# Kernel optimization log

Measured on AMD Instinct MI355X. Metric: run time of the kernel, lower is better.

Reference implementation:

```python
import jax, jax.numpy as jnp
import numpy as np

IN, HID, BATCH = 1024, 1024, 4096


def _linear_params(key, out_dim, in_dim):
    # torch.nn.Linear default init: U(-1/sqrt(in), 1/sqrt(in))
    k1, k2 = jax.random.split(key)
    bound = 1.0 / np.sqrt(in_dim)
    w = jax.random.uniform(k1, (out_dim, in_dim), jnp.float32, -bound, bound)
    b = jax.random.uniform(k2, (out_dim,), jnp.float32, -bound, bound)
    return w, b


def setup_inputs() -> dict:
    key = jax.random.key(0)
    keys = jax.random.split(key, 11)
    inp = {
        'input': jax.random.normal(keys[0], (BATCH, IN), jnp.float32),
        'h': jax.random.normal(keys[1], (BATCH, HID), jnp.float32),
        'c': jax.random.normal(keys[2], (BATCH, HID), jnp.float32),
    }
    names = ['i_i', 'i_h', 'f_i', 'f_h', 'g_i', 'g_h', 'o_i', 'o_h']
    for n, k in zip(names, keys[3:]):
        in_dim = IN if n.endswith('_i') else HID
        w, b = _linear_params(k, HID, in_dim)
        inp['w_' + n] = w
        inp['b_' + n] = b
    return inp


def reference(input, h, c,
              w_i_i, b_i_i, w_i_h, b_i_h,
              w_f_i, b_f_i, w_f_h, b_f_h,
              w_g_i, b_g_i, w_g_h, b_g_h,
              w_o_i, b_o_i, w_o_h, b_o_h):
    def lin(x, w, b):
        return x @ w.T + b

    i = jax.nn.sigmoid(lin(input, w_i_i, b_i_i) + lin(h, w_i_h, b_i_h))
    f = jax.nn.sigmoid(lin(input, w_f_i, b_f_i) + lin(h, w_f_h, b_f_h))
    g = jnp.tanh(lin(input, w_g_i, b_g_i) + lin(h, w_g_h, b_g_h))
    o = jax.nn.sigmoid(lin(input, w_o_i, b_o_i) + lin(h, w_o_h, b_o_h))
    c_prime = f * c + i * g
    h_prime = o * jnp.tanh(c_prime)
    return (h_prime, c_prime)
```

## Files before the change

kernel.cpp:

```cpp
#include <hip/hip_runtime.h>
#include <stdint.h>

#define BATCH 4096
#define IN_DIM 1024
#define HID 1024
#define KDIM 2048
#define NGATE 4096
#define EPITCH 136

typedef __attribute__((ext_vector_type(4))) float floatx4;
typedef __attribute__((ext_vector_type(8))) __bf16 bf16x8;
typedef __attribute__((ext_vector_type(8))) unsigned short ushort8;

__device__ __forceinline__ unsigned short f2bf(float f) {
    union { float f; unsigned int u; } v; v.f = f;
    unsigned int u = v.u;
    u += 0x7fffu + ((u >> 16) & 1u);
    return (unsigned short)(u >> 16);
}
__device__ __forceinline__ float bf2f(unsigned short s) {
    union { unsigned int u; float f; } v; v.u = ((unsigned int)s) << 16;
    return v.f;
}
__device__ __forceinline__ ushort8 cvt8(const float* __restrict__ src) {
    float4 v0 = ((const float4*)src)[0];
    float4 v1 = ((const float4*)src)[1];
    ushort8 o = { f2bf(v0.x), f2bf(v0.y), f2bf(v0.z), f2bf(v0.w),
                  f2bf(v1.x), f2bf(v1.y), f2bf(v1.z), f2bf(v1.w) };
    return o;
}

__global__ __launch_bounds__(256) void prep_kernel(
    const float* __restrict__ x,  const float* __restrict__ h,
    const float* __restrict__ wii, const float* __restrict__ wih,
    const float* __restrict__ wfi, const float* __restrict__ wfh,
    const float* __restrict__ wgi, const float* __restrict__ wgh,
    const float* __restrict__ woi, const float* __restrict__ woh,
    const float* __restrict__ bii, const float* __restrict__ bih,
    const float* __restrict__ bfi, const float* __restrict__ bfh,
    const float* __restrict__ bgi, const float* __restrict__ bgh,
    const float* __restrict__ boi, const float* __restrict__ boh,
    unsigned short* __restrict__ Xb,
    unsigned short* __restrict__ Wb,
    float* __restrict__ bias)
{
    const int bid = blockIdx.x;
    const int tid = threadIdx.x;

    if (bid < 2048) {
        const int e = (bid * 256 + tid) * 8;
        const int b = e >> 10, k = e & 1023;
        *(ushort8*)(Xb + (size_t)b * KDIM + k) = cvt8(x + e);
    } else if (bid < 4096) {
        const int e = ((bid - 2048) * 256 + tid) * 8;
        const int b = e >> 10, k = e & 1023;
        *(ushort8*)(Xb + (size_t)b * KDIM + 1024 + k) = cvt8(h + e);
    } else if (bid < 8192) {
        const int m   = (bid - 4096) >> 9;
        const int off = (bid - 4096) & 511;
        const int e = (off * 256 + tid) * 8;
        const int n = e >> 10, k = e & 1023;
        const float* src;
        switch (m) {
            case 0: src = wii; break; case 1: src = wih; break;
            case 2: src = wfi; break; case 3: src = wfh; break;
            case 4: src = wgi; break; case 5: src = wgh; break;
            case 6: src = woi; break; default: src = woh; break;
        }
        const int gate = m >> 1, part = m & 1;
        *(ushort8*)(Wb + (size_t)(n * 4 + gate) * KDIM + part * 1024 + k)
            = cvt8(src + e);
    } else {
        const int t = (bid - 8192) * 256 + tid;
        const int gate = (bid - 8192) >> 2;
        const int n = t & 1023;
        const float *bi, *bh_;
        switch (gate) {
            case 0: bi = bii; bh_ = bih; break;
            case 1: bi = bfi; bh_ = bfh; break;
            case 2: bi = bgi; bh_ = bgh; break;
            default: bi = boi; bh_ = boh; break;
        }
        bias[n * 4 + gate] = bi[n] + bh_[n];
    }
}

#define GLD16(g, l)                                                          \
    __builtin_amdgcn_global_load_lds(                                        \
        (__attribute__((address_space(1))) void*)(g),                        \
        (__attribute__((address_space(3))) void*)(l), 16, 0, 0)

__global__ __launch_bounds__(256) void gemm_lstm(
    const unsigned short* __restrict__ X,
    const unsigned short* __restrict__ W,
    const float* __restrict__ bias,
    const float* __restrict__ c_in,
    float* __restrict__ out)
{
    __shared__ __align__(16) unsigned char smem[128 * EPITCH * 2];
    unsigned short* As = (unsigned short*)smem;
    unsigned short* Bs = (unsigned short*)(smem + 8192);
    unsigned short* E  = (unsigned short*)smem;

    const int tid  = threadIdx.x;
    const int wave = tid >> 6;
    const int lane = tid & 63;
    const int quad = lane >> 4, idx = lane & 15;
    const int wm = (wave >> 1) * 64, wn = (wave & 1) * 64;

    const int rowA0 = blockIdx.x * 128;
    const int rowB0 = blockIdx.y * 128;

    const int srow = tid >> 2, skk = (tid & 3) * 8;
    const unsigned short* gA0 = X + (size_t)(rowA0 + srow) * KDIM + skk;
    const unsigned short* gA1 = X + (size_t)(rowA0 + 64 + srow) * KDIM + skk;
    const unsigned short* gB0 = W + (size_t)(rowB0 + srow) * KDIM + skk;
    const unsigned short* gB1 = W + (size_t)(rowB0 + 64 + srow) * KDIM + skk;

    floatx4 acc[4][4] = {};

    for (int k0 = 0; k0 < KDIM; k0 += 32) {
        GLD16(gA0 + k0, As + tid * 8);
        GLD16(gA1 + k0, As + 2048 + tid * 8);
        GLD16(gB0 + k0, Bs + tid * 8);
        GLD16(gB1 + k0, Bs + 2048 + tid * 8);
        __syncthreads();

        bf16x8 af[4], bfr[4];
#pragma unroll
        for (int i = 0; i < 4; ++i)
            af[i] = *(const bf16x8*)(As + (wm + i * 16 + idx) * 32 + quad * 8);
#pragma unroll
        for (int j = 0; j < 4; ++j)
            bfr[j] = *(const bf16x8*)(Bs + (wn + j * 16 + idx) * 32 + quad * 8);
#pragma unroll
        for (int i = 0; i < 4; ++i)
#pragma unroll
            for (int j = 0; j < 4; ++j)
                acc[i][j] = __builtin_amdgcn_mfma_f32_16x16x32_bf16(
                    af[i], bfr[j], acc[i][j], 0, 0, 0);
        __syncthreads();
    }

    const int g = idx & 3;
#pragma unroll
    for (int j = 0; j < 4; ++j) {
        const int col = wn + j * 16 + idx;
        const float bv = bias[rowB0 + col];
#pragma unroll
        for (int i = 0; i < 4; ++i) {
#pragma unroll
            for (int r = 0; r < 4; ++r) {
                const int row = wm + i * 16 + quad * 4 + r;
                const float v  = acc[i][j][r] + bv;
                const float vv = (g == 2) ? 2.f * v : v;
                const float s  = 1.f / (1.f + __expf(-vv));
                const float a  = (g == 2) ? 2.f * s - 1.f : s;
                E[row * EPITCH + col] = f2bf(a);
            }
        }
    }
    __syncthreads();

    const int tid8 = tid & 7;
    const int rowo = tid >> 3;
    float* __restrict__ out_h = out;
    float* __restrict__ out_c = out + (size_t)BATCH * HID;

#pragma unroll
    for (int p = 0; p < 4; ++p) {
        const int row_l = p * 32 + rowo;
        const int row_g = rowA0 + row_l;
        const int colc  = tid8 * 16;
        ushort8 e0 = *(const ushort8*)(E + row_l * EPITCH + colc);
        ushort8 e1 = *(const ushort8*)(E + row_l * EPITCH + colc + 8);
        const int u0 = (rowB0 >> 2) + tid8 * 4;
        const float4 cv = *(const float4*)(c_in + (size_t)row_g * HID + u0);

        float cvv[4] = { cv.x, cv.y, cv.z, cv.w };
        float hp[4], cp[4];
#pragma unroll
        for (int d = 0; d < 4; ++d) {
            const ushort8& e = (d < 2) ? e0 : e1;
            const int b = (d & 1) * 4;
            const float iv = bf2f(e[b + 0]);
            const float fv = bf2f(e[b + 1]);
            const float gv = bf2f(e[b + 2]);
            const float ov = bf2f(e[b + 3]);
            const float c2 = fv * cvv[d] + iv * gv;
            const float e2 = __expf(2.f * c2);
            cp[d] = c2;
            hp[d] = ov * ((e2 - 1.f) / (e2 + 1.f));
        }
        float4 hv = { hp[0], hp[1], hp[2], hp[3] };
        float4 cpv = { cp[0], cp[1], cp[2], cp[3] };
        *(float4*)(out_h + (size_t)row_g * HID + u0) = hv;
        *(float4*)(out_c + (size_t)row_g * HID + u0) = cpv;
    }
}

extern "C" void kernel_launch(void* const* d_in, const int* in_sizes, int n_in,
                              void* d_out, int out_size, void* d_ws, size_t ws_size,
                              hipStream_t stream) {
    const float* x   = (const float*)d_in[0];
    const float* h   = (const float*)d_in[1];
    const float* c   = (const float*)d_in[2];
    const float* wii = (const float*)d_in[3];
    const float* bii = (const float*)d_in[4];
    const float* wih = (const float*)d_in[5];
    const float* bih = (const float*)d_in[6];
    const float* wfi = (const float*)d_in[7];
    const float* bfi = (const float*)d_in[8];
    const float* wfh = (const float*)d_in[9];
    const float* bfh = (const float*)d_in[10];
    const float* wgi = (const float*)d_in[11];
    const float* bgi = (const float*)d_in[12];
    const float* wgh = (const float*)d_in[13];
    const float* bgh = (const float*)d_in[14];
    const float* woi = (const float*)d_in[15];
    const float* boi = (const float*)d_in[16];
    const float* woh = (const float*)d_in[17];
    const float* boh = (const float*)d_in[18];

    char* ws = (char*)d_ws;
    unsigned short* Xb  = (unsigned short*)ws;
    unsigned short* Wb  = (unsigned short*)(ws + ((size_t)16 << 20));
    float*          bsv = (float*)(ws + ((size_t)32 << 20));

    prep_kernel<<<8208, 256, 0, stream>>>(
        x, h, wii, wih, wfi, wfh, wgi, wgh, woi, woh,
        bii, bih, bfi, bfh, bgi, bgh, boi, boh, Xb, Wb, bsv);

    dim3 g2(BATCH / 128, NGATE / 128);
    gemm_lstm<<<g2, 256, 0, stream>>>(Xb, Wb, bsv, c, (float*)d_out);
}
```

Baseline: 242.3 us.

## Double K tile to 64 and XOR-swizzle LDS layout for fragment loads

Result: faster. 227.5 us (-6.1%).

```diff
diff --git a/kernel.cpp b/kernel.cpp
--- a/kernel.cpp
+++ b/kernel.cpp
@@ -7,6 +7,7 @@
 #define KDIM 2048
 #define NGATE 4096
 #define EPITCH 136
+#define BK 64
 
 typedef __attribute__((ext_vector_type(4))) float floatx4;
 typedef __attribute__((ext_vector_type(8))) __bf16 bf16x8;
@@ -99,7 +100,7 @@
 {
     __shared__ __align__(16) unsigned char smem[128 * EPITCH * 2];
     unsigned short* As = (unsigned short*)smem;
-    unsigned short* Bs = (unsigned short*)(smem + 8192);
+    unsigned short* Bs = (unsigned short*)(smem + 16384);
     unsigned short* E  = (unsigned short*)smem;
 
     const int tid  = threadIdx.x;
@@ -111,34 +112,43 @@
     const int rowA0 = blockIdx.x * 128;
     const int rowB0 = blockIdx.y * 128;
 
-    const int srow = tid >> 2, skk = (tid & 3) * 8;
-    const unsigned short* gA0 = X + (size_t)(rowA0 + srow) * KDIM + skk;
-    const unsigned short* gA1 = X + (size_t)(rowA0 + 64 + srow) * KDIM + skk;
-    const unsigned short* gB0 = W + (size_t)(rowB0 + srow) * KDIM + skk;
-    const unsigned short* gB1 = W + (size_t)(rowB0 + 64 + srow) * KDIM + skk;
+    const int srow = tid >> 3;
+    const int skk  = ((tid & 7) ^ (srow & 7)) * 8;
+    const unsigned short* gA = X + (size_t)(rowA0 + srow) * KDIM + skk;
+    const unsigned short* gB = W + (size_t)(rowB0 + srow) * KDIM + skk;
+    const size_t rstride = (size_t)32 * KDIM;
+
+    const int swz = (idx & 7);
 
     floatx4 acc[4][4] = {};
 
-    for (int k0 = 0; k0 < KDIM; k0 += 32) {
-        GLD16(gA0 + k0, As + tid * 8);
-        GLD16(gA1 + k0, As + 2048 + tid * 8);
-        GLD16(gB0 + k0, Bs + tid * 8);
-        GLD16(gB1 + k0, Bs + 2048 + tid * 8);
+    for (int k0 = 0; k0 < KDIM; k0 += BK) {
+#pragma unroll
+        for (int r = 0; r < 4; ++r) {
+            GLD16(gA + k0 + r * rstride, As + (r * 256 + tid) * 8);
+            GLD16(gB + k0 + r * rstride, Bs + (r * 256 + tid) * 8);
+        }
         __syncthreads();
 
-        bf16x8 af[4], bfr[4];
-#pragma unroll
-        for (int i = 0; i < 4; ++i)
-            af[i] = *(const bf16x8*)(As + (wm + i * 16 + idx) * 32 + quad * 8);
-#pragma unroll
-        for (int j = 0; j < 4; ++j)
-            bfr[j] = *(const bf16x8*)(Bs + (wn + j * 16 + idx) * 32 + quad * 8);
-#pragma unroll
-        for (int i = 0; i < 4; ++i)
+        bf16x8 af[4][2], bfr[4][2];
+#pragma unroll
+        for (int t = 0; t < 2; ++t) {
+            const int co = ((t * 4 + quad) ^ swz) * 8;
+#pragma unroll
+            for (int i = 0; i < 4; ++i)
+                af[i][t] = *(const bf16x8*)(As + (wm + i * 16 + idx) * BK + co);
 #pragma unroll
             for (int j = 0; j < 4; ++j)
-                acc[i][j] = __builtin_amdgcn_mfma_f32_16x16x32_bf16(
-                    af[i], bfr[j], acc[i][j], 0, 0, 0);
+                bfr[j][t] = *(const bf16x8*)(Bs + (wn + j * 16 + idx) * BK + co);
+        }
+#pragma unroll
+        for (int t = 0; t < 2; ++t)
+#pragma unroll
+            for (int i = 0; i < 4; ++i)
+#pragma unroll
+                for (int j = 0; j < 4; ++j)
+                    acc[i][j] = __builtin_amdgcn_mfma_f32_16x16x32_bf16(
+                        af[i][t], bfr[j][t], acc[i][j], 0, 0, 0);
         __syncthreads();
     }
 
```
